# Kernel tuning notes

Measured on AMD Instinct MI355X. Metric: run time of the kernel, lower is better.

## Reference

```python
import jax, jax.numpy as jnp
import numpy as np

B, S, E, H, R = 2, 1024, 1024, 16, 32
D = E // H  # head_dim = 64


def setup_inputs() -> dict:
    key = jax.random.key(0)
    ks = jax.random.split(key, 8)
    f = jax.random.normal
    return {
        "query": f(ks[0], (B, S, E), jnp.float32),
        "key": f(ks[1], (B, S, E), jnp.float32),  # unused by the module's forward, kept for signature fidelity
        "value": f(ks[2], (B, S, E), jnp.float32),
        "rules_keys": f(ks[3], (H, R, D), jnp.float32) * 0.02,   # nn.init.normal_(std=0.02)
        "rules_widths": jnp.ones((H, R, D), jnp.float32),
        "Wq": f(ks[4], (E, E), jnp.float32) * (E ** -0.5),
        "bq": jnp.zeros((E,), jnp.float32),
        "Wv": f(ks[5], (E * R, E), jnp.float32) * (E ** -0.5),
        "bv": jnp.zeros((E * R,), jnp.float32),
        "Wo": f(ks[6], (E, E), jnp.float32) * (E ** -0.5),
        "bo": jnp.zeros((E,), jnp.float32),
    }


def reference(query, key, value, rules_keys, rules_widths, Wq, bq, Wv, bv, Wo, bo):
    scale = D ** -0.5
    # query projection -> per-head layout (B,S,H,D)
    q = ((query @ Wq.T) + bq) * scale
    q = q.reshape(B, S, H, D)
    # fuzzy Gaussian membership: L1 distance to rule keys, scaled by widths,
    # HTSK -> mean over head_dim. z: (B,S,H,R)
    diff = jnp.abs(q[:, :, :, None, :] - rules_keys[None, None])        # (B,S,H,R,D)
    z = -0.5 * jnp.mean((diff / rules_widths[None, None]) ** 2, axis=-1)  # (B,S,H,R)
    attn = jax.nn.softmax(z, axis=-1)  # softmax over rules (dropout p=0 -> identity)
    # value projection to per-rule values: (B,S,H,R,D)
    v = ((value @ Wv.T) + bv) * scale
    v = v.reshape(B, S, H, D, R).transpose(0, 1, 2, 4, 3)
    # rule-weighted aggregation
    out = jnp.einsum('bshr,bshrd->bshd', attn, v)  # (B,S,H,D)
    # faithful to original torch code: transpose(1,2) then view(B,-1,H*D)
    # (this is a head-major flatten, reproduced exactly)
    out = out.transpose(0, 2, 1, 3).reshape(B, S, H * D)
    return (out @ Wo.T) + bo
```

## Files before the change

### kernel.cpp

```cpp
#include <hip/hip_runtime.h>
#include <hip/hip_bf16.h>
#include <cstdint>

typedef float f32x4 __attribute__((ext_vector_type(4)));
typedef short bf16x8 __attribute__((ext_vector_type(8)));

__device__ __forceinline__ unsigned short f32_to_bf16_rne(float f) {
  unsigned int u = __float_as_uint(f);
  return (unsigned short)((u + 0x7FFFu + ((u >> 16) & 1u)) >> 16);
}

#define GLOAD_LDS16(gptr, lptr)                                                             \
  __builtin_amdgcn_global_load_lds((const __attribute__((address_space(1))) unsigned int*)(gptr), \
                                   (__attribute__((address_space(3))) unsigned int*)(lptr), 16, 0, 0)

__global__ __launch_bounds__(256) void cvt_all(const float* __restrict__ wv,
                                               const float* __restrict__ q,
                                               const float* __restrict__ v,
                                               const float* __restrict__ wq,
                                               const float* __restrict__ wo,
                                               unsigned short* __restrict__ wvb,
                                               unsigned short* __restrict__ qb,
                                               unsigned short* __restrict__ vb,
                                               unsigned short* __restrict__ wqb,
                                               unsigned short* __restrict__ wob) {
  int i = blockIdx.x * 256 + threadIdx.x;
  const float* src;
  unsigned short* dst;
  int off;
  if (i < 4194304)      { src = wv; dst = wvb; off = i; }
  else if (i < 4456448) { src = q;  dst = qb;  off = i - 4194304; }
  else if (i < 4718592) { src = v;  dst = vb;  off = i - 4456448; }
  else if (i < 4849664) { src = wq; dst = wqb; off = i - 4718592; }
  else                  { src = wo; dst = wob; off = i - 4849664; }
  const float4* s = (const float4*)src;
  float4 a = s[2 * off], b = s[2 * off + 1];
  uint4 o;
  o.x = (unsigned)f32_to_bf16_rne(a.x) | ((unsigned)f32_to_bf16_rne(a.y) << 16);
  o.y = (unsigned)f32_to_bf16_rne(a.z) | ((unsigned)f32_to_bf16_rne(a.w) << 16);
  o.z = (unsigned)f32_to_bf16_rne(b.x) | ((unsigned)f32_to_bf16_rne(b.y) << 16);
  o.w = (unsigned)f32_to_bf16_rne(b.z) | ((unsigned)f32_to_bf16_rne(b.w) << 16);
  ((uint4*)dst)[off] = o;
}

__global__ __launch_bounds__(256) void fuzzy2_k(const float* __restrict__ qf,
                                                const float* __restrict__ rk,
                                                const float* __restrict__ rw,
                                                float* __restrict__ attn) {
  __shared__ float lk[32][65];
  __shared__ float lc[32][65];
  const int tid = threadIdx.x;
  const int h = blockIdx.y;
  const int mbase = blockIdx.x * 128;

  for (int idx = tid; idx < 2048; idx += 256) {
    int r = idx >> 6, d = idx & 63;
    lk[r][d] = rk[(size_t)(h * 32 + r) * 64 + d];
    float w = rw[(size_t)(h * 32 + r) * 64 + d];
    lc[r][d] = 0.0078125f / (w * w);
  }
  __syncthreads();

  const int g = tid >> 5;
  const int r = tid & 31;
#pragma unroll 1
  for (int it = 0; it < 16; ++it) {
    int m = mbase + it * 8 + g;
    const float* qrow = qf + (size_t)m * 1024 + h * 64;
    float acc = 0.f;
#pragma unroll
    for (int d0 = 0; d0 < 64; d0 += 4) {
      float4 q4 = *(const float4*)(qrow + d0);
      const float* qp = (const float*)&q4;
#pragma unroll
      for (int j = 0; j < 4; ++j) {
        float diff = qp[j] - lk[r][d0 + j];
        acc += lc[r][d0 + j] * diff * diff;
      }
    }
    float z = -acc;
    float mx = z;
#pragma unroll
    for (int mask = 16; mask >= 1; mask >>= 1) mx = fmaxf(mx, __shfl_xor(mx, mask));
    float e = __expf(z - mx);
    float s = e;
#pragma unroll
    for (int mask = 16; mask >= 1; mask >>= 1) s += __shfl_xor(s, mask);
    attn[(size_t)m * 512 + h * 32 + r] = e / s;
  }
}

__global__ __launch_bounds__(256) void gemm_bt64(const unsigned short* __restrict__ A,
                                                 const unsigned short* __restrict__ W,
                                                 const float* __restrict__ bias, float scale,
                                                 int M, int N, int K, float* __restrict__ Cf) {
  constexpr int BK = 32;
  __shared__ unsigned short As[2][64 * BK];
  __shared__ unsigned short Bs[2][64 * BK];
  const int tid = threadIdx.x;
  const int wid = tid >> 6;
  const int lane = tid & 63;
  const int l15 = lane & 15;
  const int l4 = lane >> 4;
  const int bm = blockIdx.y * 64;
  const int bn = blockIdx.x * 64;
  const int wr = (wid >> 1) * 32;
  const int wc = (wid & 1) * 32;

  f32x4 acc[2][2];
#pragma unroll
  for (int i = 0; i < 2; ++i)
#pragma unroll
    for (int j = 0; j < 2; ++j) acc[i][j] = (f32x4){0.f, 0.f, 0.f, 0.f};

  const int nk = K / BK;
  auto stage = [&](int buf, int kt) {
    int c = tid;
    int row = c >> 2, ch = c & 3;
    int sch = ch ^ ((row >> 1) & 3);
    GLOAD_LDS16(A + (size_t)(bm + row) * K + kt * BK + sch * 8, &As[buf][c * 8]);
    GLOAD_LDS16(W + (size_t)(bn + row) * K + kt * BK + sch * 8, &Bs[buf][c * 8]);
  };

  stage(0, 0);
  __syncthreads();

  for (int kt = 0; kt < nk; ++kt) {
    const int cur = kt & 1;
    if (kt + 1 < nk) stage(cur ^ 1, kt + 1);
    bf16x8 a[2], b[2];
#pragma unroll
    for (int mi = 0; mi < 2; ++mi) {
      int rl = wr + mi * 16 + l15;
      int ph = (rl * 64 + l4 * 16) ^ ((((unsigned)rl >> 1) & 3) << 4);
      a[mi] = *(const bf16x8*)((const char*)&As[cur][0] + ph);
    }
#pragma unroll
    for (int ni = 0; ni < 2; ++ni) {
      int rl = wc + ni * 16 + l15;
      int ph = (rl * 64 + l4 * 16) ^ ((((unsigned)rl >> 1) & 3) << 4);
      b[ni] = *(const bf16x8*)((const char*)&Bs[cur][0] + ph);
    }
#pragma unroll
    for (int mi = 0; mi < 2; ++mi)
#pragma unroll
      for (int ni = 0; ni < 2; ++ni)
        acc[mi][ni] = __builtin_amdgcn_mfma_f32_16x16x32_bf16(a[mi], b[ni], acc[mi][ni], 0, 0, 0);
    __syncthreads();
  }

#pragma unroll
  for (int mi = 0; mi < 2; ++mi) {
#pragma unroll
    for (int ni = 0; ni < 2; ++ni) {
      int gm = bm + wr + mi * 16 + l4 * 4;
      int gn = bn + wc + ni * 16 + l15;
      float bval = bias[gn];
#pragma unroll
      for (int q = 0; q < 4; ++q)
        Cf[(size_t)(gm + q) * N + gn] = (acc[mi][ni][q] + bval) * scale;
    }
  }
}

__global__ __launch_bounds__(512) void gemm2_k(const unsigned short* __restrict__ A,
                                               const unsigned short* __restrict__ W,
                                               const float* __restrict__ bias, float scale,
                                               const float* __restrict__ attn,
                                               unsigned short* __restrict__ X) {
  constexpr int K = 1024, BK = 32, NK = K / BK;
  extern __shared__ unsigned short lds[];
  unsigned short* Asl = lds;
  unsigned short* Bsl = lds + 4 * 8192;
  const int tid = threadIdx.x;
  const int wid = tid >> 6, lane = tid & 63;
  const int l15 = lane & 15, l4 = lane >> 4;
  const int wm = wid >> 2, wn = wid & 3;

  int orig = blockIdx.x;
  int swz = (orig & 7) * 128 + (orig >> 3);
  const int bm = (swz & 7) * 256, bn = (swz >> 3) * 256;

  auto stageA = [&](int buf, int kt) {
#pragma unroll
    for (int i = 0; i < 2; ++i) {
      int c = i * 512 + tid;
      int row = c >> 2, ch = c & 3;
      int sch = ch ^ ((row >> 1) & 3);
      GLOAD_LDS16(A + (size_t)(bm + row) * K + kt * BK + sch * 8, Asl + buf * 8192 + c * 8);
    }
  };
  auto stageB = [&](int buf, int kt) {
#pragma unroll
    for (int i = 0; i < 2; ++i) {
      int c = i * 512 + tid;
      int row = c >> 2, ch = c & 3;
      int sch = ch ^ ((row >> 1) & 3);
      GLOAD_LDS16(W + (size_t)(bn + row) * K + kt * BK + sch * 8, Bsl + buf * 8192 + c * 8);
    }
  };

  f32x4 acc[8][4];
#pragma unroll
  for (int i = 0; i < 8; ++i)
#pragma unroll
    for (int j = 0; j < 4; ++j) acc[i][j] = (f32x4){0.f, 0.f, 0.f, 0.f};

  bf16x8 a0[8], a1[8], b0[4], b1[4];

#define FRAG_PH(rl) (((rl) * 64 + l4 * 16) ^ ((((unsigned)(rl) >> 1) & 3) << 4))

#define BODY(aC, aN, bC, bN, Tt, DO_STAGE, WN)                                            \
  do {                                                                                    \
    if (DO_STAGE) { stageA(((Tt) + 2) & 3, (Tt) + 2); stageB(((Tt) + 2) & 3, (Tt) + 2); } \
    asm volatile("s_waitcnt vmcnt(" #WN ")" ::: "memory");                                \
    __builtin_amdgcn_s_barrier();                                                         \
    {                                                                                     \
      const char* _ab = (const char*)(Asl + (((Tt) + 1) & 3) * 8192);                     \
      const char* _bb = (const char*)(Bsl + (((Tt) + 1) & 3) * 8192);                     \
      __builtin_amdgcn_s_setprio(1);                                                      \
      _Pragma("unroll") for (int mf = 0; mf < 8; ++mf) {                                  \
        _Pragma("unroll") for (int nf = 0; nf < 4; ++nf)                                  \
          acc[mf][nf] =                                                                   \
              __builtin_amdgcn_mfma_f32_16x16x32_bf16(aC[mf], bC[nf], acc[mf][nf], 0, 0, 0); \
        if (mf < 4) {                                                                     \
          aN[mf] = *(const bf16x8*)(_ab + FRAG_PH(wm * 128 + mf * 16 + l15));             \
          bN[mf] = *(const bf16x8*)(_bb + FRAG_PH(wn * 64 + mf * 16 + l15));              \
        } else if (mf < 6) {                                                              \
          int i0 = 2 * mf - 4, i1 = 2 * mf - 3;                                           \
          aN[i0] = *(const bf16x8*)(_ab + FRAG_PH(wm * 128 + i0 * 16 + l15));             \
          aN[i1] = *(const bf16x8*)(_ab + FRAG_PH(wm * 128 + i1 * 16 + l15));             \
        }                                                                                 \
      }                                                                                   \
      __builtin_amdgcn_s_setprio(0);                                                      \
    }                                                                                     \
    asm volatile("s_waitcnt lgkmcnt(0)" ::: "memory");                                    \
    __builtin_amdgcn_sched_barrier(0);                                                    \
  } while (0)

  stageA(0, 0); stageB(0, 0);
  stageA(1, 1); stageB(1, 1);
  asm volatile("s_waitcnt vmcnt(4)" ::: "memory");
  __builtin_amdgcn_s_barrier();
#pragma unroll
  for (int nf = 0; nf < 4; ++nf)
    b0[nf] = *(const bf16x8*)((const char*)Bsl + FRAG_PH(wn * 64 + nf * 16 + l15));
#pragma unroll
  for (int mf = 0; mf < 8; ++mf)
    a0[mf] = *(const bf16x8*)((const char*)Asl + FRAG_PH(wm * 128 + mf * 16 + l15));
  asm volatile("s_waitcnt lgkmcnt(0)" ::: "memory");
  __builtin_amdgcn_sched_barrier(0);

  for (int T = 0; T < 30; T += 2) {
    BODY(a0, a1, b0, b1, T, 1, 4);
    BODY(a1, a0, b1, b0, (T + 1), 1, 4);
  }
  BODY(a0, a1, b0, b1, 30, 0, 0);
  __builtin_amdgcn_s_setprio(1);
#pragma unroll
  for (int mf = 0; mf < 8; ++mf)
#pragma unroll
    for (int nf = 0; nf < 4; ++nf)
      acc[mf][nf] = __builtin_amdgcn_mfma_f32_16x16x32_bf16(a1[mf], b1[nf], acc[mf][nf], 0, 0, 0);
  __builtin_amdgcn_s_setprio(0);
#undef BODY
#undef FRAG_PH

  const int h = bn >> 11;
  const int dbase = ((bn & 2047) + wn * 64) >> 5;
#pragma unroll
  for (int mf = 0; mf < 8; ++mf) {
    int gm0 = bm + wm * 128 + mf * 16 + l4 * 4;
    float red[4][2];
#pragma unroll
    for (int q = 0; q < 4; ++q) { red[q][0] = 0.f; red[q][1] = 0.f; }
#pragma unroll
    for (int nf = 0; nf < 4; ++nf) {
      int col = bn + wn * 64 + nf * 16 + l15;
      float bval = bias[col];
      int r = (nf & 1) * 16 + l15;
      int g = nf >> 1;
#pragma unroll
      for (int q = 0; q < 4; ++q) {
        float w = attn[(size_t)(gm0 + q) * 512 + h * 32 + r];
        red[q][g] += (acc[mf][nf][q] + bval) * w;
      }
    }
#pragma unroll
    for (int q = 0; q < 4; ++q)
#pragma unroll
      for (int g = 0; g < 2; ++g) {
        float vv = red[q][g];
        for (int mask = 1; mask < 16; mask <<= 1) vv += __shfl_xor(vv, mask);
        red[q][g] = vv * scale;
      }
    if (l15 == 0) {
#pragma unroll
      for (int q = 0; q < 4; ++q) {
        int m = gm0 + q;
        int bb = m >> 10, s = m & 1023;
        size_t base = (((size_t)(bb * 16 + h)) * 1024 + s) * 64;
        unsigned lo = f32_to_bf16_rne(red[q][0]);
        unsigned hi = f32_to_bf16_rne(red[q][1]);
        ((unsigned*)X)[(base + dbase) >> 1] = lo | (hi << 16);
      }
    }
  }
}

extern "C" void kernel_launch(void* const* d_in, const int* in_sizes, int n_in, void* d_out,
                              int out_size, void* d_ws, size_t ws_size, hipStream_t stream) {
  const float* query = (const float*)d_in[0];
  const float* value = (const float*)d_in[2];
  const float* rk = (const float*)d_in[3];
  const float* rw = (const float*)d_in[4];
  const float* Wq = (const float*)d_in[5];
  const float* bq = (const float*)d_in[6];
  const float* Wv = (const float*)d_in[7];
  const float* bv = (const float*)d_in[8];
  const float* Wo = (const float*)d_in[9];
  const float* bo = (const float*)d_in[10];
  float* out = (float*)d_out;

  const float scale = 0.125f;

  char* p = (char*)d_ws;
  unsigned short* Wv_b = (unsigned short*)p; p += (size_t)33554432 * 2;
  unsigned short* Aq_b = (unsigned short*)p; p += (size_t)2097152 * 2;
  unsigned short* Av_b = (unsigned short*)p; p += (size_t)2097152 * 2;
  unsigned short* Wq_b = (unsigned short*)p; p += (size_t)1048576 * 2;
  unsigned short* Wo_b = (unsigned short*)p; p += (size_t)1048576 * 2;
  float* qf = (float*)p;   p += (size_t)2097152 * 4;
  float* attn = (float*)p; p += (size_t)1048576 * 4;
  unsigned short* X = (unsigned short*)p;

  cvt_all<<<19456, 256, 0, stream>>>(Wv, query, value, Wq, Wo, Wv_b, Aq_b, Av_b, Wq_b, Wo_b);

  gemm_bt64<<<dim3(16, 32), 256, 0, stream>>>(Aq_b, Wq_b, bq, scale, 2048, 1024, 1024, qf);
  fuzzy2_k<<<dim3(16, 16), 256, 0, stream>>>(qf, rk, rw, attn);
  hipFuncSetAttribute((const void*)gemm2_k, hipFuncAttributeMaxDynamicSharedMemorySize, 131072);
  gemm2_k<<<1024, 512, 131072, stream>>>(Av_b, Wv_b, bv, scale, attn, X);
  gemm_bt64<<<dim3(16, 32), 256, 0, stream>>>(X, Wo_b, bo, 1.0f, 2048, 1024, 1024, out);
}
```

Baseline: 232.0 us.

## Restructure gemm2 main loop into two-phase half-tile MFMA with split staging

Replaces the double-buffered register fragment pipeline (a0/a1, b0/b1 with loads interleaved into MFMA) with a two-phase schedule per K-tile. Each phase loads half the A fragments, issues one operand's global-to-LDS staging, synchronises with barriers and runs 16 MFMAs. Register use drops by half the fragment buffers, which could raise occupancy or reduce spills. The cost is extra barriers per K-tile and less overlap between LDS reads and MFMA issue.

Measured after the change: 236.6 us. 1.02x slower.

```diff
diff --git a/kernel.cpp b/kernel.cpp
--- a/kernel.cpp
+++ b/kernel.cpp
@@ -168,7 +168,7 @@
                                                const float* __restrict__ bias, float scale,
                                                const float* __restrict__ attn,
                                                unsigned short* __restrict__ X) {
-  constexpr int K = 1024, BK = 32, NK = K / BK;
+  constexpr int K = 1024, BK = 32;
   extern __shared__ unsigned short lds[];
   unsigned short* Asl = lds;
   unsigned short* Bsl = lds + 4 * 8192;
@@ -206,64 +206,66 @@
 #pragma unroll
     for (int j = 0; j < 4; ++j) acc[i][j] = (f32x4){0.f, 0.f, 0.f, 0.f};
 
-  bf16x8 a0[8], a1[8], b0[4], b1[4];
+  bf16x8 a[4], b[4];
 
 #define FRAG_PH(rl) (((rl) * 64 + l4 * 16) ^ ((((unsigned)(rl) >> 1) & 3) << 4))
 
-#define BODY(aC, aN, bC, bN, Tt, DO_STAGE, WN)                                            \
+#define PHASE0(CB, SB, KT, DO_ST)                                                         \
   do {                                                                                    \
-    if (DO_STAGE) { stageA(((Tt) + 2) & 3, (Tt) + 2); stageB(((Tt) + 2) & 3, (Tt) + 2); } \
+    const char* _ab = (const char*)(Asl + (CB) * 8192);                                   \
+    const char* _bb = (const char*)(Bsl + (CB) * 8192);                                   \
+    _Pragma("unroll") for (int nf = 0; nf < 4; ++nf)                                      \
+      b[nf] = *(const bf16x8*)(_bb + FRAG_PH(wn * 64 + nf * 16 + l15));                   \
+    _Pragma("unroll") for (int mf = 0; mf < 4; ++mf)                                      \
+      a[mf] = *(const bf16x8*)(_ab + FRAG_PH(wm * 128 + mf * 16 + l15));                  \
+    if (DO_ST) stageA(SB, KT);                                                            \
+    __builtin_amdgcn_s_barrier();                                                         \
+    asm volatile("s_waitcnt lgkmcnt(0)" ::: "memory");                                    \
+    __builtin_amdgcn_sched_barrier(0);                                                    \
+    __builtin_amdgcn_s_setprio(1);                                                        \
+    _Pragma("unroll") for (int mf = 0; mf < 4; ++mf)                                      \
+      _Pragma("unroll") for (int nf = 0; nf < 4; ++nf)                                    \
+        acc[mf][nf] =                                                                     \
+            __builtin_amdgcn_mfma_f32_16x16x32_bf16(a[mf], b[nf], acc[mf][nf], 0, 0, 0);  \
+    __builtin_amdgcn_s_setprio(0);                                                        \
+    __builtin_amdgcn_s_barrier();                                                         \
+  } while (0)
+
+#define PHASE1(CB, SB, KT, DO_ST, WN)                                                     \
+  do {                                                                                    \
+    const char* _ab = (const char*)(Asl + (CB) * 8192);                                   \
+    _Pragma("unroll") for (int mf = 0; mf < 4; ++mf)                                      \
+      a[mf] = *(const bf16x8*)(_ab + FRAG_PH(wm * 128 + 64 + mf * 16 + l15));             \
+    if (DO_ST) stageB(SB, KT);                                                            \
     asm volatile("s_waitcnt vmcnt(" #WN ")" ::: "memory");                                \
     __builtin_amdgcn_s_barrier();                                                         \
-    {                                                                                     \
-      const char* _ab = (const char*)(Asl + (((Tt) + 1) & 3) * 8192);                     \
-      const char* _bb = (const char*)(Bsl + (((Tt) + 1) & 3) * 8192);                     \
-      __builtin_amdgcn_s_setprio(1);                                                      \
-      _Pragma("unroll") for (int mf = 0; mf < 8; ++mf) {                                  \
-        _Pragma("unroll") for (int nf = 0; nf < 4; ++nf)                                  \
-          acc[mf][nf] =                                                                   \
-              __builtin_amdgcn_mfma_f32_16x16x32_bf16(aC[mf], bC[nf], acc[mf][nf], 0, 0, 0); \
-        if (mf < 4) {                                                                     \
-          aN[mf] = *(const bf16x8*)(_ab + FRAG_PH(wm * 128 + mf * 16 + l15));             \
-          bN[mf] = *(const bf16x8*)(_bb + FRAG_PH(wn * 64 + mf * 16 + l15));              \
-        } else if (mf < 6) {                                                              \
-          int i0 = 2 * mf - 4, i1 = 2 * mf - 3;                                           \
-          aN[i0] = *(const bf16x8*)(_ab + FRAG_PH(wm * 128 + i0 * 16 + l15));             \
-          aN[i1] = *(const bf16x8*)(_ab + FRAG_PH(wm * 128 + i1 * 16 + l15));             \
-        }                                                                                 \
-      }                                                                                   \
-      __builtin_amdgcn_s_setprio(0);                                                      \
-    }                                                                                     \
     asm volatile("s_waitcnt lgkmcnt(0)" ::: "memory");                                    \
     __builtin_amdgcn_sched_barrier(0);                                                    \
+    __builtin_amdgcn_s_setprio(1);                                                        \
+    _Pragma("unroll") for (int mf = 0; mf < 4; ++mf)                                      \
+      _Pragma("unroll") for (int nf = 0; nf < 4; ++nf)                                    \
+        acc[4 + mf][nf] =                                                                 \
+            __builtin_amdgcn_mfma_f32_16x16x32_bf16(a[mf], b[nf], acc[4 + mf][nf], 0, 0, 0); \
+    __builtin_amdgcn_s_setprio(0);                                                        \
+    __builtin_amdgcn_s_barrier();                                                         \
   } while (0)
 
   stageA(0, 0); stageB(0, 0);
   stageA(1, 1); stageB(1, 1);
   asm volatile("s_waitcnt vmcnt(4)" ::: "memory");
   __builtin_amdgcn_s_barrier();
-#pragma unroll
-  for (int nf = 0; nf < 4; ++nf)
-    b0[nf] = *(const bf16x8*)((const char*)Bsl + FRAG_PH(wn * 64 + nf * 16 + l15));
-#pragma unroll
-  for (int mf = 0; mf < 8; ++mf)
-    a0[mf] = *(const bf16x8*)((const char*)Asl + FRAG_PH(wm * 128 + mf * 16 + l15));
-  asm volatile("s_waitcnt lgkmcnt(0)" ::: "memory");
-  __builtin_amdgcn_sched_barrier(0);
-
-  for (int T = 0; T < 30; T += 2) {
-    BODY(a0, a1, b0, b1, T, 1, 4);
-    BODY(a1, a0, b1, b0, (T + 1), 1, 4);
-  }
-  BODY(a0, a1, b0, b1, 30, 0, 0);
-  __builtin_amdgcn_s_setprio(1);
-#pragma unroll
-  for (int mf = 0; mf < 8; ++mf)
-#pragma unroll
-    for (int nf = 0; nf < 4; ++nf)
-      acc[mf][nf] = __builtin_amdgcn_mfma_f32_16x16x32_bf16(a1[mf], b1[nf], acc[mf][nf], 0, 0, 0);
-  __builtin_amdgcn_s_setprio(0);
-#undef BODY
+
+  for (int T = 0; T < 30; ++T) {
+    const int cb = T & 3, sb = (T + 2) & 3;
+    PHASE0(cb, sb, T + 2, 1);
+    PHASE1(cb, sb, T + 2, 1, 4);
+  }
+  PHASE0(2, 0, 0, 0);
+  PHASE1(2, 0, 0, 0, 0);
+  PHASE0(3, 0, 0, 0);
+  PHASE1(3, 0, 0, 0, 0);
+#undef PHASE0
+#undef PHASE1
 #undef FRAG_PH
 
   const int h = bn >> 11;
```

## Switch value-projection GEMM to 32x32x16 MFMA tiles with new fragment layout

Applied to the files above, without the earlier changes.

Replaces the 16x16x32 bf16 MFMA tiling in the fused value-projection/rule-aggregation kernel with 32x32x16 MFMA, reorganising accumulators, LDS fragment loads and the epilogue. The larger MFMA shape is meant to cut LDS fragment traffic and instruction count per FLOP. The epilogue now reduces over 32 rules with a 5-step shuffle per output element, which may add cross-lane shuffle cost and more scattered attn loads.

New measurement: 343.0 us. +47.8%, slower.

```diff
diff --git a/kernel.cpp b/kernel.cpp
--- a/kernel.cpp
+++ b/kernel.cpp
@@ -3,6 +3,7 @@
 #include <cstdint>
 
 typedef float f32x4 __attribute__((ext_vector_type(4)));
+typedef float f32x16 __attribute__((ext_vector_type(16)));
 typedef short bf16x8 __attribute__((ext_vector_type(8)));
 
 __device__ __forceinline__ unsigned short f32_to_bf16_rne(float f) {
@@ -168,13 +169,13 @@
                                                const float* __restrict__ bias, float scale,
                                                const float* __restrict__ attn,
                                                unsigned short* __restrict__ X) {
-  constexpr int K = 1024, BK = 32, NK = K / BK;
+  constexpr int K = 1024, BK = 32;
   extern __shared__ unsigned short lds[];
   unsigned short* Asl = lds;
   unsigned short* Bsl = lds + 4 * 8192;
   const int tid = threadIdx.x;
   const int wid = tid >> 6, lane = tid & 63;
-  const int l15 = lane & 15, l4 = lane >> 4;
+  const int l31 = lane & 31, lh = lane >> 5;
   const int wm = wid >> 2, wn = wid & 3;
 
   int orig = blockIdx.x;
@@ -200,15 +201,15 @@
     }
   };
 
-  f32x4 acc[8][4];
-#pragma unroll
-  for (int i = 0; i < 8; ++i)
-#pragma unroll
-    for (int j = 0; j < 4; ++j) acc[i][j] = (f32x4){0.f, 0.f, 0.f, 0.f};
-
-  bf16x8 a0[8], a1[8], b0[4], b1[4];
-
-#define FRAG_PH(rl) (((rl) * 64 + l4 * 16) ^ ((((unsigned)(rl) >> 1) & 3) << 4))
+  f32x16 acc[4][2];
+#pragma unroll
+  for (int i = 0; i < 4; ++i)
+#pragma unroll
+    for (int j = 0; j < 2; ++j) acc[i][j] = (f32x16)(0.f);
+
+  bf16x8 a0[4][2], a1[4][2], b0[2][2], b1[2][2];
+
+#define PH32(rl, ch) ((((rl) * 64) + (ch) * 16) ^ ((((unsigned)(rl) >> 1) & 3) << 4))
 
 #define BODY(aC, aN, bC, bN, Tt, DO_STAGE, WN)                                            \
   do {                                                                                    \
@@ -219,19 +220,25 @@
       const char* _ab = (const char*)(Asl + (((Tt) + 1) & 3) * 8192);                     \
       const char* _bb = (const char*)(Bsl + (((Tt) + 1) & 3) * 8192);                     \
       __builtin_amdgcn_s_setprio(1);                                                      \
-      _Pragma("unroll") for (int mf = 0; mf < 8; ++mf) {                                  \
-        _Pragma("unroll") for (int nf = 0; nf < 4; ++nf)                                  \
-          acc[mf][nf] =                                                                   \
-              __builtin_amdgcn_mfma_f32_16x16x32_bf16(aC[mf], bC[nf], acc[mf][nf], 0, 0, 0); \
-        if (mf < 4) {                                                                     \
-          aN[mf] = *(const bf16x8*)(_ab + FRAG_PH(wm * 128 + mf * 16 + l15));             \
-          bN[mf] = *(const bf16x8*)(_bb + FRAG_PH(wn * 64 + mf * 16 + l15));              \
-        } else if (mf < 6) {                                                              \
-          int i0 = 2 * mf - 4, i1 = 2 * mf - 3;                                           \
-          aN[i0] = *(const bf16x8*)(_ab + FRAG_PH(wm * 128 + i0 * 16 + l15));             \
-          aN[i1] = *(const bf16x8*)(_ab + FRAG_PH(wm * 128 + i1 * 16 + l15));             \
+      _Pragma("unroll") for (int rb = 0; rb < 4; ++rb)                                    \
+        _Pragma("unroll") for (int cb = 0; cb < 2; ++cb) {                                \
+          acc[rb][cb] = __builtin_amdgcn_mfma_f32_32x32x16_bf16(aC[rb][0], bC[cb][0],     \
+                                                                acc[rb][cb], 0, 0, 0);    \
+          int i = rb * 2 + cb;                                                            \
+          aN[i >> 1][i & 1] =                                                             \
+              *(const bf16x8*)(_ab + PH32(wm * 128 + (i >> 1) * 32 + l31,                 \
+                                          (i & 1) * 2 + lh));                             \
         }                                                                                 \
-      }                                                                                   \
+      _Pragma("unroll") for (int rb = 0; rb < 4; ++rb)                                    \
+        _Pragma("unroll") for (int cb = 0; cb < 2; ++cb) {                                \
+          acc[rb][cb] = __builtin_amdgcn_mfma_f32_32x32x16_bf16(aC[rb][1], bC[cb][1],     \
+                                                                acc[rb][cb], 0, 0, 0);    \
+          int i = rb * 2 + cb;                                                            \
+          if (i < 4)                                                                      \
+            bN[i >> 1][i & 1] =                                                           \
+                *(const bf16x8*)(_bb + PH32(wn * 64 + (i >> 1) * 32 + l31,                \
+                                            (i & 1) * 2 + lh));                           \
+        }                                                                                 \
       __builtin_amdgcn_s_setprio(0);                                                      \
     }                                                                                     \
     asm volatile("s_waitcnt lgkmcnt(0)" ::: "memory");                                    \
@@ -243,11 +250,15 @@
   asm volatile("s_waitcnt vmcnt(4)" ::: "memory");
   __builtin_amdgcn_s_barrier();
 #pragma unroll
-  for (int nf = 0; nf < 4; ++nf)
-    b0[nf] = *(const bf16x8*)((const char*)Bsl + FRAG_PH(wn * 64 + nf * 16 + l15));
-#pragma unroll
-  for (int mf = 0; mf < 8; ++mf)
-    a0[mf] = *(const bf16x8*)((const char*)Asl + FRAG_PH(wm * 128 + mf * 16 + l15));
+  for (int cb = 0; cb < 2; ++cb)
+#pragma unroll
+    for (int kh = 0; kh < 2; ++kh)
+      b0[cb][kh] = *(const bf16x8*)((const char*)Bsl + PH32(wn * 64 + cb * 32 + l31, kh * 2 + lh));
+#pragma unroll
+  for (int rb = 0; rb < 4; ++rb)
+#pragma unroll
+    for (int kh = 0; kh < 2; ++kh)
+      a0[rb][kh] = *(const bf16x8*)((const char*)Asl + PH32(wm * 128 + rb * 32 + l31, kh * 2 + lh));
   asm volatile("s_waitcnt lgkmcnt(0)" ::: "memory");
   __builtin_amdgcn_sched_barrier(0);
 
@@ -258,50 +269,40 @@
   BODY(a0, a1, b0, b1, 30, 0, 0);
   __builtin_amdgcn_s_setprio(1);
 #pragma unroll
-  for (int mf = 0; mf < 8; ++mf)
-#pragma unroll
-    for (int nf = 0; nf < 4; ++nf)
-      acc[mf][nf] = __builtin_amdgcn_mfma_f32_16x16x32_bf16(a1[mf], b1[nf], acc[mf][nf], 0, 0, 0);
+  for (int kh = 0; kh < 2; ++kh)
+#pragma unroll
+    for (int rb = 0; rb < 4; ++rb)
+#pragma unroll
+      for (int cb = 0; cb < 2; ++cb)
+        acc[rb][cb] = __builtin_amdgcn_mfma_f32_32x32x16_bf16(a1[rb][kh], b1[cb][kh],
+                                                              acc[rb][cb], 0, 0, 0);
   __builtin_amdgcn_s_setprio(0);
 #undef BODY
-#undef FRAG_PH
+#undef PH32
 
   const int h = bn >> 11;
   const int dbase = ((bn & 2047) + wn * 64) >> 5;
-#pragma unroll
-  for (int mf = 0; mf < 8; ++mf) {
-    int gm0 = bm + wm * 128 + mf * 16 + l4 * 4;
-    float red[4][2];
-#pragma unroll
-    for (int q = 0; q < 4; ++q) { red[q][0] = 0.f; red[q][1] = 0.f; }
-#pragma unroll
-    for (int nf = 0; nf < 4; ++nf) {
-      int col = bn + wn * 64 + nf * 16 + l15;
-      float bval = bias[col];
-      int r = (nf & 1) * 16 + l15;
-      int g = nf >> 1;
-#pragma unroll
-      for (int q = 0; q < 4; ++q) {
-        float w = attn[(size_t)(gm0 + q) * 512 + h * 32 + r];
-        red[q][g] += (acc[mf][nf][q] + bval) * w;
+  const float bv0 = bias[bn + wn * 64 + l31];
+  const float bv1 = bias[bn + wn * 64 + 32 + l31];
+#pragma unroll
+  for (int rb = 0; rb < 4; ++rb) {
+    const int m0 = bm + wm * 128 + rb * 32 + 4 * lh;
+#pragma unroll
+    for (int reg = 0; reg < 16; ++reg) {
+      int m = m0 + (reg & 3) + 8 * (reg >> 2);
+      float w = attn[(size_t)m * 512 + h * 32 + l31];
+      float v0 = (acc[rb][0][reg] + bv0) * w;
+      float v1 = (acc[rb][1][reg] + bv1) * w;
+#pragma unroll
+      for (int mask = 1; mask < 32; mask <<= 1) {
+        v0 += __shfl_xor(v0, mask);
+        v1 += __shfl_xor(v1, mask);
       }
-    }
-#pragma unroll
-    for (int q = 0; q < 4; ++q)
-#pragma unroll
-      for (int g = 0; g < 2; ++g) {
-        float vv = red[q][g];
-        for (int mask = 1; mask < 16; mask <<= 1) vv += __shfl_xor(vv, mask);
-        red[q][g] = vv * scale;
-      }
-    if (l15 == 0) {
-#pragma unroll
-      for (int q = 0; q < 4; ++q) {
-        int m = gm0 + q;
+      if (l31 == 0) {
         int bb = m >> 10, s = m & 1023;
         size_t base = (((size_t)(bb * 16 + h)) * 1024 + s) * 64;
-        unsigned lo = f32_to_bf16_rne(red[q][0]);
-        unsigned hi = f32_to_bf16_rne(red[q][1]);
+        unsigned lo = f32_to_bf16_rne(v0 * scale);
+        unsigned hi = f32_to_bf16_rne(v1 * scale);
         ((unsigned*)X)[(base + dbase) >> 1] = lo | (hi << 16);
       }
     }
```

## Fuse Wv fp32-to-bf16 conversion into value-projection GEMM loader

Applied to the files above, without the earlier changes.

Removes the separate pass that converted the large per-rule value weight to bf16 in workspace; the GEMM now loads fp32 weights into registers, converts them and writes bf16 into LDS inside the pipelined K loop. This avoids writing and re-reading a 64MB bf16 copy plus a dedicated conversion launch. In exchange the GEMM loses direct global-to-LDS loads for B, reads twice the bytes per weight tile, and adds conversion ALU and LDS stores to its main loop.

After: 256.6 us. 10.6% more time.

```diff
diff --git a/kernel.cpp b/kernel.cpp
--- a/kernel.cpp
+++ b/kernel.cpp
@@ -14,12 +14,10 @@
   __builtin_amdgcn_global_load_lds((const __attribute__((address_space(1))) unsigned int*)(gptr), \
                                    (__attribute__((address_space(3))) unsigned int*)(lptr), 16, 0, 0)
 
-__global__ __launch_bounds__(256) void cvt_all(const float* __restrict__ wv,
-                                               const float* __restrict__ q,
+__global__ __launch_bounds__(256) void cvt_all(const float* __restrict__ q,
                                                const float* __restrict__ v,
                                                const float* __restrict__ wq,
                                                const float* __restrict__ wo,
-                                               unsigned short* __restrict__ wvb,
                                                unsigned short* __restrict__ qb,
                                                unsigned short* __restrict__ vb,
                                                unsigned short* __restrict__ wqb,
@@ -28,11 +26,10 @@
   const float* src;
   unsigned short* dst;
   int off;
-  if (i < 4194304)      { src = wv; dst = wvb; off = i; }
-  else if (i < 4456448) { src = q;  dst = qb;  off = i - 4194304; }
-  else if (i < 4718592) { src = v;  dst = vb;  off = i - 4456448; }
-  else if (i < 4849664) { src = wq; dst = wqb; off = i - 4718592; }
-  else                  { src = wo; dst = wob; off = i - 4849664; }
+  if (i < 262144)      { src = q;  dst = qb;  off = i; }
+  else if (i < 524288) { src = v;  dst = vb;  off = i - 262144; }
+  else if (i < 655360) { src = wq; dst = wqb; off = i - 524288; }
+  else                 { src = wo; dst = wob; off = i - 655360; }
   const float4* s = (const float4*)src;
   float4 a = s[2 * off], b = s[2 * off + 1];
   uint4 o;
@@ -164,11 +161,11 @@
 }
 
 __global__ __launch_bounds__(512) void gemm2_k(const unsigned short* __restrict__ A,
-                                               const unsigned short* __restrict__ W,
+                                               const float* __restrict__ W32,
                                                const float* __restrict__ bias, float scale,
                                                const float* __restrict__ attn,
                                                unsigned short* __restrict__ X) {
-  constexpr int K = 1024, BK = 32, NK = K / BK;
+  constexpr int K = 1024, BK = 32;
   extern __shared__ unsigned short lds[];
   unsigned short* Asl = lds;
   unsigned short* Bsl = lds + 4 * 8192;
@@ -190,15 +187,6 @@
       GLOAD_LDS16(A + (size_t)(bm + row) * K + kt * BK + sch * 8, Asl + buf * 8192 + c * 8);
     }
   };
-  auto stageB = [&](int buf, int kt) {
-#pragma unroll
-    for (int i = 0; i < 2; ++i) {
-      int c = i * 512 + tid;
-      int row = c >> 2, ch = c & 3;
-      int sch = ch ^ ((row >> 1) & 3);
-      GLOAD_LDS16(W + (size_t)(bn + row) * K + kt * BK + sch * 8, Bsl + buf * 8192 + c * 8);
-    }
-  };
 
   f32x4 acc[8][4];
 #pragma unroll
@@ -207,13 +195,42 @@
     for (int j = 0; j < 4; ++j) acc[i][j] = (f32x4){0.f, 0.f, 0.f, 0.f};
 
   bf16x8 a0[8], a1[8], b0[4], b1[4];
-
-#define FRAG_PH(rl) (((rl) * 64 + l4 * 16) ^ ((((unsigned)(rl) >> 1) & 3) << 4))
-
-#define BODY(aC, aN, bC, bN, Tt, DO_STAGE, WN)                                            \
+  float4 g00, g01, g10, g11;
+
+#define FRAG_PH(rl) (((rl) * 64 + l4 * 16) ^ ((((unsigned)rl >> 1) & 3) << 4))
+#define PKR(lo, hi) ((unsigned)f32_to_bf16_rne(lo) | ((unsigned)f32_to_bf16_rne(hi) << 16))
+
+#define LOAD_B32(KT)                                                                      \
   do {                                                                                    \
-    if (DO_STAGE) { stageA(((Tt) + 2) & 3, (Tt) + 2); stageB(((Tt) + 2) & 3, (Tt) + 2); } \
+    int _c = tid, _row = _c >> 2, _sch = (_c & 3) ^ ((_row >> 1) & 3);                    \
+    const float* _s0 = W32 + (size_t)(bn + _row) * 1024 + (KT) * 32 + _sch * 8;           \
+    g00 = *(const float4*)_s0;                                                            \
+    g01 = *(const float4*)(_s0 + 4);                                                      \
+    _c = tid + 512; _row = _c >> 2; _sch = (_c & 3) ^ ((_row >> 1) & 3);                  \
+    const float* _s1 = W32 + (size_t)(bn + _row) * 1024 + (KT) * 32 + _sch * 8;           \
+    g10 = *(const float4*)_s1;                                                            \
+    g11 = *(const float4*)(_s1 + 4);                                                      \
+  } while (0)
+
+#define CVT_B(Tt)                                                                         \
+  do {                                                                                    \
+    asm volatile("s_waitcnt vmcnt(2)" ::: "memory");                                      \
+    unsigned short* _dst = Bsl + (((Tt) + 1) & 3) * 8192;                                 \
+    uint4 _p0, _p1;                                                                       \
+    _p0.x = PKR(g00.x, g00.y); _p0.y = PKR(g00.z, g00.w);                                 \
+    _p0.z = PKR(g01.x, g01.y); _p0.w = PKR(g01.z, g01.w);                                 \
+    _p1.x = PKR(g10.x, g10.y); _p1.y = PKR(g10.z, g10.w);                                 \
+    _p1.z = PKR(g11.x, g11.y); _p1.w = PKR(g11.z, g11.w);                                 \
+    *reinterpret_cast<uint4*>(_dst + tid * 8) = _p0;                                      \
+    *reinterpret_cast<uint4*>(_dst + (tid + 512) * 8) = _p1;                              \
+  } while (0)
+
+#define BODY(aC, aN, bC, bN, Tt, HAS_CVT, DO_STAGE, WN)                                   \
+  do {                                                                                    \
+    if (HAS_CVT) CVT_B(Tt);                                                               \
+    if (DO_STAGE) { LOAD_B32((Tt) + 2); stageA(((Tt) + 2) & 3, (Tt) + 2); }               \
     asm volatile("s_waitcnt vmcnt(" #WN ")" ::: "memory");                                \
+    asm volatile("s_waitcnt lgkmcnt(0)" ::: "memory");                                    \
     __builtin_amdgcn_s_barrier();                                                         \
     {                                                                                     \
       const char* _ab = (const char*)(Asl + (((Tt) + 1) & 3) * 8192);                     \
@@ -238,9 +255,13 @@
     __builtin_amdgcn_sched_barrier(0);                                                    \
   } while (0)
 
-  stageA(0, 0); stageB(0, 0);
-  stageA(1, 1); stageB(1, 1);
-  asm volatile("s_waitcnt vmcnt(4)" ::: "memory");
+  LOAD_B32(0);
+  stageA(0, 0);
+  CVT_B(-1);
+  LOAD_B32(1);
+  stageA(1, 1);
+  CVT_B(0);
+  asm volatile("s_waitcnt lgkmcnt(0)" ::: "memory");
   __builtin_amdgcn_s_barrier();
 #pragma unroll
   for (int nf = 0; nf < 4; ++nf)
@@ -251,11 +272,13 @@
   asm volatile("s_waitcnt lgkmcnt(0)" ::: "memory");
   __builtin_amdgcn_sched_barrier(0);
 
-  for (int T = 0; T < 30; T += 2) {
-    BODY(a0, a1, b0, b1, T, 1, 4);
-    BODY(a1, a0, b1, b0, (T + 1), 1, 4);
-  }
-  BODY(a0, a1, b0, b1, 30, 0, 0);
+  BODY(a0, a1, b0, b1, 0, 0, 1, 6);
+  for (int T = 1; T < 29; T += 2) {
+    BODY(a1, a0, b1, b0, T, 1, 1, 6);
+    BODY(a0, a1, b0, b1, T + 1, 1, 1, 6);
+  }
+  BODY(a1, a0, b1, b0, 29, 1, 1, 6);
+  BODY(a0, a1, b0, b1, 30, 1, 0, 0);
   __builtin_amdgcn_s_setprio(1);
 #pragma unroll
   for (int mf = 0; mf < 8; ++mf)
@@ -264,6 +287,8 @@
       acc[mf][nf] = __builtin_amdgcn_mfma_f32_16x16x32_bf16(a1[mf], b1[nf], acc[mf][nf], 0, 0, 0);
   __builtin_amdgcn_s_setprio(0);
 #undef BODY
+#undef CVT_B
+#undef LOAD_B32
 #undef FRAG_PH
 
   const int h = bn >> 11;
@@ -325,7 +350,6 @@
   const float scale = 0.125f;
 
   char* p = (char*)d_ws;
-  unsigned short* Wv_b = (unsigned short*)p; p += (size_t)33554432 * 2;
   unsigned short* Aq_b = (unsigned short*)p; p += (size_t)2097152 * 2;
   unsigned short* Av_b = (unsigned short*)p; p += (size_t)2097152 * 2;
   unsigned short* Wq_b = (unsigned short*)p; p += (size_t)1048576 * 2;
@@ -334,11 +358,11 @@
   float* attn = (float*)p; p += (size_t)1048576 * 4;
   unsigned short* X = (unsigned short*)p;
 
-  cvt_all<<<19456, 256, 0, stream>>>(Wv, query, value, Wq, Wo, Wv_b, Aq_b, Av_b, Wq_b, Wo_b);
+  cvt_all<<<3072, 256, 0, stream>>>(query, value, Wq, Wo, Aq_b, Av_b, Wq_b, Wo_b);
 
   gemm_bt64<<<dim3(16, 32), 256, 0, stream>>>(Aq_b, Wq_b, bq, scale, 2048, 1024, 1024, qf);
   fuzzy2_k<<<dim3(16, 16), 256, 0, stream>>>(qf, rk, rw, attn);
   hipFuncSetAttribute((const void*)gemm2_k, hipFuncAttributeMaxDynamicSharedMemorySize, 131072);
-  gemm2_k<<<1024, 512, 131072, stream>>>(Av_b, Wv_b, bv, scale, attn, X);
+  gemm2_k<<<1024, 512, 131072, stream>>>(Av_b, Wv, bv, scale, attn, X);
   gemm_bt64<<<dim3(16, 32), 256, 0, stream>>>(X, Wo_b, bo, 1.0f, 2048, 1024, 1024, out);
 }
```
